# Kernel optimization log

Hardware: AMD Instinct MI355X
Metric: run time of the kernel (lower is better)

The kernel has to match this reference:

```python
import jax, jax.numpy as jnp
import numpy as np

B, C, D, N, R = 64, 768, 14, 64, 32  # batch, channels, spatial d, num_outputs, rank

def setup_inputs() -> dict:
    key = jax.random.key(0)
    k1, k2, k3 = jax.random.split(key, 3)
    X = jax.random.normal(k1, (B, C, D, D), dtype=jnp.float32)
    Y = jax.random.normal(k2, (B, C, D, D), dtype=jnp.float32)
    w = jax.random.normal(k3, (2, N, C, R), dtype=jnp.float32) * 0.05
    b = jnp.zeros((N,), dtype=jnp.float32)
    return {"X": X, "Y": Y, "w": w, "b": b}

def reference(X, Y, w, b):
    d = X.shape[-1]
    d2 = d * d
    Xf = X.reshape(X.shape[0], X.shape[1], d2)  # [B, C, d^2]
    Yf = Y.reshape(Y.shape[0], Y.shape[1], d2)  # [B, C, d^2]
    # T1 = X^T w0 -> [B, N, d^2, R]; T2^T = Y^T w1 -> [B, N, d^2, R]
    # trace(T1 @ T2) = sum(T1 * T2^T) elementwise (same math as original)
    T1 = jnp.einsum('bcp,ncr->bnpr', Xf, w[0])
    T2t = jnp.einsum('bcp,ncr->bnpr', Yf, w[1])
    z = jnp.einsum('bnpr,bnpr->bn', T1, T2t) / d2 + b  # [B, N]
    return jax.nn.softmax(z, axis=-1)
```

## Files before the change

### kernel.cpp

```cpp
#include <hip/hip_runtime.h>
#include <hip/hip_bf16.h>


typedef float f32x4 __attribute__((ext_vector_type(4)));
typedef __bf16 bf16x8 __attribute__((ext_vector_type(8)));
typedef __bf16 bf16x4 __attribute__((ext_vector_type(4)));

#define KFLAT ((size_t)(768 * 768))
#define LDP 40

__global__ __launch_bounds__(256) void gram_v4(
    const float* __restrict__ X, const float* __restrict__ Y,
    const float* __restrict__ w0, const float* __restrict__ w1,
    __bf16* __restrict__ Mout, __bf16* __restrict__ Wout)
{
    const int t    = threadIdx.x;
    const int lane = t & 63;
    const int wid  = t >> 6;
    const int wr   = wid >> 1, wc = wid & 1;
    const int lr   = lane & 15, lq = lane >> 4;

    const bool wmode = (blockIdx.x >= 2304);
    int bx, bat, lda, nfull, tail;
    const float *A, *B;
    __bf16* Out;
    float scale;
    if (!wmode) {
        const int orig = (blockIdx.x & 7) * 288 + (blockIdx.x >> 3);
        bat = orig / 36; bx = orig % 36;
        A = X + (size_t)bat * (768 * 196);
        B = Y + (size_t)bat * (768 * 196);
        Out = Mout; lda = 196; nfull = 6; tail = 1; scale = 1.0f / 196.0f;
    } else {
        const int wbid = blockIdx.x - 2304;
        bat = wbid / 36; bx = wbid % 36;
        A = w0 + (size_t)bat * (768 * 32);
        B = w1 + (size_t)bat * (768 * 32);
        Out = Wout; lda = 32; nfull = 1; tail = 0; scale = 1.0f;
    }
    const int c0 = (bx / 6) * 128, cc0 = (bx % 6) * 128;

    __shared__ __bf16 As[128][LDP];
    __shared__ __bf16 Bs[128][LDP];

    const int r = t >> 1;
    const int h = t & 1;
    const float* Ap = A + (size_t)(c0  + r) * lda + h * 16;
    const float* Bp = B + (size_t)(cc0 + r) * lda + h * 16;

    f32x4 acc[4][4];
#pragma unroll
    for (int i = 0; i < 4; ++i)
#pragma unroll
        for (int j = 0; j < 4; ++j) acc[i][j] = (f32x4){0.f, 0.f, 0.f, 0.f};

    auto stage = [&](const f32x4* va, const f32x4* vb) {
        bf16x8 u;
#pragma unroll
        for (int e = 0; e < 4; ++e) { u[e] = (__bf16)va[0][e]; u[e+4] = (__bf16)va[1][e]; }
        *(bf16x8*)&As[r][h * 16] = u;
#pragma unroll
        for (int e = 0; e < 4; ++e) { u[e] = (__bf16)va[2][e]; u[e+4] = (__bf16)va[3][e]; }
        *(bf16x8*)&As[r][h * 16 + 8] = u;
#pragma unroll
        for (int e = 0; e < 4; ++e) { u[e] = (__bf16)vb[0][e]; u[e+4] = (__bf16)vb[1][e]; }
        *(bf16x8*)&Bs[r][h * 16] = u;
#pragma unroll
        for (int e = 0; e < 4; ++e) { u[e] = (__bf16)vb[2][e]; u[e+4] = (__bf16)vb[3][e]; }
        *(bf16x8*)&Bs[r][h * 16 + 8] = u;
    };

    auto compute = [&]() {
        bf16x8 af[4], bfr[4];
#pragma unroll
        for (int m = 0; m < 4; ++m) af[m]  = *(const bf16x8*)&As[wr * 64 + m * 16 + lr][lq * 8];
#pragma unroll
        for (int n = 0; n < 4; ++n) bfr[n] = *(const bf16x8*)&Bs[wc * 64 + n * 16 + lr][lq * 8];
#pragma unroll
        for (int m = 0; m < 4; ++m)
#pragma unroll
            for (int n = 0; n < 4; ++n)
                acc[m][n] = __builtin_amdgcn_mfma_f32_16x16x32_bf16(af[m], bfr[n], acc[m][n], 0, 0, 0);
    };

    f32x4 pa[4], pb[4], na[4], nb[4];
#pragma unroll
    for (int j = 0; j < 4; ++j) {
        pa[j] = *(const f32x4*)(Ap + j * 4); pb[j] = *(const f32x4*)(Bp + j * 4);
        na[j] = (f32x4){0.f, 0.f, 0.f, 0.f}; nb[j] = (f32x4){0.f, 0.f, 0.f, 0.f};
    }

    for (int kk = 0; kk < nfull; ++kk) {
        __syncthreads();
        stage(pa, pb);
        if (kk + 1 < nfull) {
            const int o = (kk + 1) * 32;
#pragma unroll
            for (int j = 0; j < 4; ++j) { na[j] = *(const f32x4*)(Ap + o + j * 4); nb[j] = *(const f32x4*)(Bp + o + j * 4); }
        }
        __syncthreads();
        compute();
#pragma unroll
        for (int j = 0; j < 4; ++j) { pa[j] = na[j]; pb[j] = nb[j]; }
    }

    if (tail) {
        __syncthreads();
        const int tr = t & 127;
        const float* src = (t < 128) ? (A + (size_t)(c0  + tr) * lda + nfull * 32)
                                     : (B + (size_t)(cc0 + tr) * lda + nfull * 32);
        f32x4 v = *(const f32x4*)src;
        __bf16* dst = (t < 128) ? &As[tr][0] : &Bs[tr][0];
        bf16x4 q4 = { (__bf16)v.x, (__bf16)v.y, (__bf16)v.z, (__bf16)v.w };
        bf16x4 z4; bf16x8 z8;
#pragma unroll
        for (int e = 0; e < 4; ++e) z4[e] = (__bf16)0.0f;
#pragma unroll
        for (int e = 0; e < 8; ++e) z8[e] = (__bf16)0.0f;
        *(bf16x4*)dst        = q4;
        *(bf16x4*)(dst + 4)  = z4;
        *(bf16x8*)(dst + 8)  = z8;
        *(bf16x8*)(dst + 16) = z8;
        *(bf16x8*)(dst + 24) = z8;
        __syncthreads();
        compute();
    }

    __bf16* Ob = Out + (size_t)bat * KFLAT + (size_t)bx * 16384 + wid * 4096 + lane * 8;
#pragma unroll
    for (int p = 0; p < 8; ++p) {
        const int f0 = p * 2, f1 = f0 + 1;
        const f32x4 u0 = acc[f0 >> 2][f0 & 3];
        const f32x4 u1 = acc[f1 >> 2][f1 & 3];
        bf16x8 o;
#pragma unroll
        for (int e = 0; e < 4; ++e) { o[e] = (__bf16)(u0[e] * scale); o[e + 4] = (__bf16)(u1[e] * scale); }
        *(bf16x8*)(Ob + p * 512) = o;
    }
}

__global__ __launch_bounds__(64) void zpartial(
    const __bf16* __restrict__ M, const __bf16* __restrict__ W,
    float* __restrict__ P, int steps)
{
    const int lane = threadIdx.x;
    const int lr = lane & 15, lq = lane >> 4;
    const size_t KK = KFLAT;

    f32x4 acc[4][4];
#pragma unroll
    for (int i = 0; i < 4; ++i)
#pragma unroll
        for (int j = 0; j < 4; ++j) acc[i][j] = (f32x4){0.f, 0.f, 0.f, 0.f};

    const size_t s0 = (size_t)blockIdx.x * steps;
    for (int s = 0; s < steps; ++s) {
        const size_t k = (s0 + s) * 32 + (size_t)lq * 8;
        bf16x8 a[4], b[4];
#pragma unroll
        for (int i = 0; i < 4; ++i) a[i] = *(const bf16x8*)(M + (size_t)(i * 16 + lr) * KK + k);
#pragma unroll
        for (int j = 0; j < 4; ++j) b[j] = *(const bf16x8*)(W + (size_t)(j * 16 + lr) * KK + k);
#pragma unroll
        for (int i = 0; i < 4; ++i)
#pragma unroll
            for (int j = 0; j < 4; ++j)
                acc[i][j] = __builtin_amdgcn_mfma_f32_16x16x32_bf16(a[i], b[j], acc[i][j], 0, 0, 0);
    }

    float* Pb = P + (size_t)blockIdx.x * 4096;
#pragma unroll
    for (int i = 0; i < 4; ++i)
#pragma unroll
        for (int j = 0; j < 4; ++j)
#pragma unroll
            for (int e = 0; e < 4; ++e) {
                const int row = i * 16 + lq * 4 + e;
                const int col = j * 16 + lr;
                Pb[row * 64 + col] = acc[i][j][e];
            }
}

__global__ __launch_bounds__(1024) void finalize(
    const float* __restrict__ P, const float* __restrict__ bias,
    float* __restrict__ out, int nchunks)
{
    __shared__ float red[16][64];
    const int b = blockIdx.x, n = threadIdx.x & 63, q = threadIdx.x >> 6;
    const int iters = nchunks >> 4;
    const float* p = P + (size_t)q * 4096 + b * 64 + n;
    float s = 0.f;
#pragma unroll 8
    for (int c = 0; c < iters; ++c) s += p[(size_t)c * 16 * 4096];
    red[q][n] = s;
    __syncthreads();
    if (q == 0) {
        float z = bias[n];
#pragma unroll
        for (int i = 0; i < 16; ++i) z += red[i][n];
        float mx = z;
#pragma unroll
        for (int off = 32; off; off >>= 1) mx = fmaxf(mx, __shfl_xor(mx, off));
        float e = __expf(z - mx);
        float den = e;
#pragma unroll
        for (int off = 32; off; off >>= 1) den += __shfl_xor(den, off);
        out[b * 64 + n] = e / den;
    }
}

extern "C" void kernel_launch(void* const* d_in, const int* in_sizes, int n_in,
                              void* d_out, int out_size, void* d_ws, size_t ws_size,
                              hipStream_t stream) {
    const float* X    = (const float*)d_in[0];
    const float* Y    = (const float*)d_in[1];
    const float* w    = (const float*)d_in[2];
    const float* bias = (const float*)d_in[3];
    float* out = (float*)d_out;

    char* ws = (char*)d_ws;
    __bf16* Mws = (__bf16*)ws;
    __bf16* Wws = (__bf16*)(ws + 75497472);
    float*  Pws = (float*)(ws + 150994944);

    const float* w0 = w;
    const float* w1 = w + (size_t)64 * 768 * 32;

    gram_v4<<<4608, 256, 0, stream>>>(X, Y, w0, w1, Mws, Wws);
    zpartial<<<1024, 64, 0, stream>>>(Mws, Wws, Pws, 18);
    finalize<<<64, 1024, 0, stream>>>(Pws, bias, out, 1024);
}
```

Baseline: 215.5 us.

## Precast inputs to padded bf16 in a separate kernel before the Gram GEMM

Adds a precast kernel that converts X, Y and w to bf16 and pads rows from 196 to 224 elements, so the Gram kernel loads bf16 directly with 16-byte vector loads, runs seven uniform K-steps and no longer needs a tail path. The Gram kernel also prefetches two K-steps ahead in registers. The aim is to halve the load traffic inside the GEMM and remove in-loop conversion work. The cost is an extra launch plus a full read of the fp32 inputs and a write of the bf16 copies. Pws aliases the Xb region, which is safe only because zpartial runs after gram.

```diff
diff --git a/kernel.cpp b/kernel.cpp
--- a/kernel.cpp
+++ b/kernel.cpp
@@ -9,9 +9,40 @@
 #define KFLAT ((size_t)(768 * 768))
 #define LDP 40
 
-__global__ __launch_bounds__(256) void gram_v4(
+__global__ __launch_bounds__(256) void precast(
     const float* __restrict__ X, const float* __restrict__ Y,
-    const float* __restrict__ w0, const float* __restrict__ w1,
+    const float* __restrict__ w,
+    __bf16* __restrict__ Xb, __bf16* __restrict__ Yb,
+    __bf16* __restrict__ w01b)
+{
+    const int id = blockIdx.x * 256 + threadIdx.x;
+    if (id < 5505024) {
+        const int half = id / 2752512;
+        const int rid  = id - half * 2752512;
+        const int row  = rid / 56;
+        const int ch   = rid - row * 56;
+        __bf16* dst = (half ? Yb : Xb) + (size_t)row * 224 + ch * 4;
+        bf16x4 o;
+        if (ch < 49) {
+            const float* src = (half ? Y : X) + (size_t)row * 196 + ch * 4;
+            f32x4 v = *(const f32x4*)src;
+            o[0] = (__bf16)v.x; o[1] = (__bf16)v.y; o[2] = (__bf16)v.z; o[3] = (__bf16)v.w;
+        } else {
+#pragma unroll
+            for (int e = 0; e < 4; ++e) o[e] = (__bf16)0.0f;
+        }
+        *(bf16x4*)dst = o;
+    } else {
+        const int wid2 = id - 5505024;
+        f32x4 v = *(const f32x4*)(w + (size_t)wid2 * 4);
+        bf16x4 o = { (__bf16)v.x, (__bf16)v.y, (__bf16)v.z, (__bf16)v.w };
+        *(bf16x4*)(w01b + (size_t)wid2 * 4) = o;
+    }
+}
+
+__global__ __launch_bounds__(256) void gram_v5(
+    const __bf16* __restrict__ Xb, const __bf16* __restrict__ Yb,
+    const __bf16* __restrict__ w01b,
     __bf16* __restrict__ Mout, __bf16* __restrict__ Wout)
 {
     const int t    = threadIdx.x;
@@ -21,22 +52,22 @@
     const int lr   = lane & 15, lq = lane >> 4;
 
     const bool wmode = (blockIdx.x >= 2304);
-    int bx, bat, lda, nfull, tail;
-    const float *A, *B;
+    int bx, bat, lda, nfull;
+    const __bf16 *A, *B;
     __bf16* Out;
     float scale;
     if (!wmode) {
         const int orig = (blockIdx.x & 7) * 288 + (blockIdx.x >> 3);
         bat = orig / 36; bx = orig % 36;
-        A = X + (size_t)bat * (768 * 196);
-        B = Y + (size_t)bat * (768 * 196);
-        Out = Mout; lda = 196; nfull = 6; tail = 1; scale = 1.0f / 196.0f;
+        A = Xb + (size_t)bat * (768 * 224);
+        B = Yb + (size_t)bat * (768 * 224);
+        Out = Mout; lda = 224; nfull = 7; scale = 1.0f / 196.0f;
     } else {
         const int wbid = blockIdx.x - 2304;
         bat = wbid / 36; bx = wbid % 36;
-        A = w0 + (size_t)bat * (768 * 32);
-        B = w1 + (size_t)bat * (768 * 32);
-        Out = Wout; lda = 32; nfull = 1; tail = 0; scale = 1.0f;
+        A = w01b + (size_t)bat * (768 * 32);
+        B = w01b + (size_t)(64 * 768 * 32) + (size_t)bat * (768 * 32);
+        Out = Wout; lda = 32; nfull = 1; scale = 1.0f;
     }
     const int c0 = (bx / 6) * 128, cc0 = (bx % 6) * 128;
 
@@ -45,30 +76,14 @@
 
     const int r = t >> 1;
     const int h = t & 1;
-    const float* Ap = A + (size_t)(c0  + r) * lda + h * 16;
-    const float* Bp = B + (size_t)(cc0 + r) * lda + h * 16;
+    const __bf16* Ap = A + (size_t)(c0  + r) * lda + h * 16;
+    const __bf16* Bp = B + (size_t)(cc0 + r) * lda + h * 16;
 
     f32x4 acc[4][4];
 #pragma unroll
     for (int i = 0; i < 4; ++i)
 #pragma unroll
         for (int j = 0; j < 4; ++j) acc[i][j] = (f32x4){0.f, 0.f, 0.f, 0.f};
-
-    auto stage = [&](const f32x4* va, const f32x4* vb) {
-        bf16x8 u;
-#pragma unroll
-        for (int e = 0; e < 4; ++e) { u[e] = (__bf16)va[0][e]; u[e+4] = (__bf16)va[1][e]; }
-        *(bf16x8*)&As[r][h * 16] = u;
-#pragma unroll
-        for (int e = 0; e < 4; ++e) { u[e] = (__bf16)va[2][e]; u[e+4] = (__bf16)va[3][e]; }
-        *(bf16x8*)&As[r][h * 16 + 8] = u;
-#pragma unroll
-        for (int e = 0; e < 4; ++e) { u[e] = (__bf16)vb[0][e]; u[e+4] = (__bf16)vb[1][e]; }
-        *(bf16x8*)&Bs[r][h * 16] = u;
-#pragma unroll
-        for (int e = 0; e < 4; ++e) { u[e] = (__bf16)vb[2][e]; u[e+4] = (__bf16)vb[3][e]; }
-        *(bf16x8*)&Bs[r][h * 16 + 8] = u;
-    };
 
     auto compute = [&]() {
         bf16x8 af[4], bfr[4];
@@ -83,47 +98,30 @@
                 acc[m][n] = __builtin_amdgcn_mfma_f32_16x16x32_bf16(af[m], bfr[n], acc[m][n], 0, 0, 0);
     };
 
-    f32x4 pa[4], pb[4], na[4], nb[4];
-#pragma unroll
-    for (int j = 0; j < 4; ++j) {
-        pa[j] = *(const f32x4*)(Ap + j * 4); pb[j] = *(const f32x4*)(Bp + j * 4);
-        na[j] = (f32x4){0.f, 0.f, 0.f, 0.f}; nb[j] = (f32x4){0.f, 0.f, 0.f, 0.f};
-    }
+    auto ld = [&](int kk, bf16x8& x0, bf16x8& x1, bf16x8& y0, bf16x8& y1) {
+        x0 = *(const bf16x8*)(Ap + kk * 32);
+        x1 = *(const bf16x8*)(Ap + kk * 32 + 8);
+        y0 = *(const bf16x8*)(Bp + kk * 32);
+        y1 = *(const bf16x8*)(Bp + kk * 32 + 8);
+    };
+
+    bf16x8 a0, a1, b0, b1, n0, n1, n2, n3, t0, t1, t2, t3;
+    ld(0, a0, a1, b0, b1);
+    if (nfull > 1) ld(1, n0, n1, n2, n3);
+    else { n0 = a0; n1 = a1; n2 = b0; n3 = b1; }
+    t0 = a0; t1 = a1; t2 = b0; t3 = b1;
 
     for (int kk = 0; kk < nfull; ++kk) {
         __syncthreads();
-        stage(pa, pb);
-        if (kk + 1 < nfull) {
-            const int o = (kk + 1) * 32;
-#pragma unroll
-            for (int j = 0; j < 4; ++j) { na[j] = *(const f32x4*)(Ap + o + j * 4); nb[j] = *(const f32x4*)(Bp + o + j * 4); }
-        }
+        *(bf16x8*)&As[r][h * 16]     = a0;
+        *(bf16x8*)&As[r][h * 16 + 8] = a1;
+        *(bf16x8*)&Bs[r][h * 16]     = b0;
+        *(bf16x8*)&Bs[r][h * 16 + 8] = b1;
+        if (kk + 2 < nfull) ld(kk + 2, t0, t1, t2, t3);
         __syncthreads();
         compute();
-#pragma unroll
-        for (int j = 0; j < 4; ++j) { pa[j] = na[j]; pb[j] = nb[j]; }
-    }
-
-    if (tail) {
-        __syncthreads();
-        const int tr = t & 127;
-        const float* src = (t < 128) ? (A + (size_t)(c0  + tr) * lda + nfull * 32)
-                                     : (B + (size_t)(cc0 + tr) * lda + nfull * 32);
-        f32x4 v = *(const f32x4*)src;
-        __bf16* dst = (t < 128) ? &As[tr][0] : &Bs[tr][0];
-        bf16x4 q4 = { (__bf16)v.x, (__bf16)v.y, (__bf16)v.z, (__bf16)v.w };
-        bf16x4 z4; bf16x8 z8;
-#pragma unroll
-        for (int e = 0; e < 4; ++e) z4[e] = (__bf16)0.0f;
-#pragma unroll
-        for (int e = 0; e < 8; ++e) z8[e] = (__bf16)0.0f;
-        *(bf16x4*)dst        = q4;
-        *(bf16x4*)(dst + 4)  = z4;
-        *(bf16x8*)(dst + 8)  = z8;
-        *(bf16x8*)(dst + 16) = z8;
-        *(bf16x8*)(dst + 24) = z8;
-        __syncthreads();
-        compute();
+        a0 = n0; a1 = n1; b0 = n2; b1 = n3;
+        n0 = t0; n1 = t1; n2 = t2; n3 = t3;
     }
 
     __bf16* Ob = Out + (size_t)bat * KFLAT + (size_t)bx * 16384 + wid * 4096 + lane * 8;
@@ -219,14 +217,15 @@
     float* out = (float*)d_out;
 
     char* ws = (char*)d_ws;
-    __bf16* Mws = (__bf16*)ws;
-    __bf16* Wws = (__bf16*)(ws + 75497472);
-    float*  Pws = (float*)(ws + 150994944);
-
-    const float* w0 = w;
-    const float* w1 = w + (size_t)64 * 768 * 32;
-
-    gram_v4<<<4608, 256, 0, stream>>>(X, Y, w0, w1, Mws, Wws);
+    __bf16* Mws  = (__bf16*)ws;
+    __bf16* Wws  = (__bf16*)(ws + 75497472);
+    float*  Pws  = (float*)(ws + 150994944);
+    __bf16* Xbws = (__bf16*)(ws + 150994944);
+    __bf16* Ybws = (__bf16*)(ws + 173015040);
+    __bf16* wbws = (__bf16*)(ws + 195035136);
+
+    precast<<<24576, 256, 0, stream>>>(X, Y, w, Xbws, Ybws, wbws);
+    gram_v5<<<4608, 256, 0, stream>>>(Xbws, Ybws, wbws, Mws, Wws);
     zpartial<<<1024, 64, 0, stream>>>(Mws, Wws, Pws, 18);
     finalize<<<64, 1024, 0, stream>>>(Pws, bias, out, 1024);
 }
```

Result: faster. 201.4 us (-6.5%).
